# Kernel optimization log

Hardware: AMD Instinct MI355X
Metric: run time of the kernel (lower is better)

The kernel has to match this reference:

```python
import jax, jax.numpy as jnp
import numpy as np

N_NODES = 50000
N_EDGES = 800000
IN_F = 191
H1, C1 = 16, 16   # conv1: heads=16, out=16, concat -> 256
H2, C2 = 8, 3     # conv2: heads=8, out=3, concat=False -> mean


def _glorot(key, shape):
    fan = shape[0] + shape[-1] if len(shape) == 2 else sum(shape)
    s = jnp.sqrt(6.0 / fan)
    return jax.random.uniform(key, shape, jnp.float32, -s, s)


def setup_inputs() -> dict:
    key = jax.random.key(0)
    ks = jax.random.split(key, 16)
    x = jax.random.normal(ks[0], (N_NODES, IN_F), jnp.float32)
    edge_index = jax.random.randint(ks[1], (2, N_EDGES), 0, N_NODES)
    edge_attr = jax.random.normal(ks[2], (N_EDGES, 1), jnp.float32)
    return {
        "x": x, "edge_index": edge_index, "edge_attr": edge_attr,
        "W1": _glorot(ks[3], (IN_F, H1 * C1)),
        "We1": _glorot(ks[4], (1, H1 * C1)),
        "a_src1": _glorot(ks[5], (H1, C1)),
        "a_dst1": _glorot(ks[6], (H1, C1)),
        "a_edge1": _glorot(ks[7], (H1, C1)),
        "b1": jnp.zeros((H1 * C1,), jnp.float32),
        "W2": _glorot(ks[8], (H1 * C1, H2 * C2)),
        "We2": _glorot(ks[9], (1, H2 * C2)),
        "a_src2": _glorot(ks[10], (H2, C2)),
        "a_dst2": _glorot(ks[11], (H2, C2)),
        "a_edge2": _glorot(ks[12], (H2, C2)),
        "b2": jnp.zeros((C2,), jnp.float32),
    }


def gat_conv(x, src, dst, edge_attr, W, We, a_src, a_dst, a_edge, bias, H, C, concat):
    # x: [N, F]; src/dst: [E'] (self loops already appended); edge_attr: [E', De]
    N = x.shape[0]
    xl = (x @ W).reshape(N, H, C)                       # [N,H,C]
    e = (edge_attr @ We).reshape(-1, H, C)              # [E',H,C]
    alpha_src = (xl * a_src).sum(-1)                    # [N,H]
    alpha_dst = (xl * a_dst).sum(-1)                    # [N,H]
    alpha_e = (e * a_edge).sum(-1)                      # [E',H]
    alpha = alpha_src[src] + alpha_dst[dst] + alpha_e   # [E',H]
    alpha = jax.nn.leaky_relu(alpha, 0.2)
    # softmax over incoming edges per destination node
    m = jax.ops.segment_max(alpha, dst, num_segments=N)
    alpha = jnp.exp(alpha - m[dst])
    den = jax.ops.segment_sum(alpha, dst, num_segments=N)
    alpha = alpha / (den[dst] + 1e-16)
    out = jax.ops.segment_sum(alpha[:, :, None] * xl[src], dst, num_segments=N)  # [N,H,C]
    if concat:
        return out.reshape(N, H * C) + bias
    return out.mean(axis=1) + bias


def reference(x, edge_index, edge_attr, W1, We1, a_src1, a_dst1, a_edge1, b1,
              W2, We2, a_src2, a_dst2, a_edge2, b2):
    N = x.shape[0]
    # add self loops (PyG default, edge_attr fill_value='mean')
    loop = jnp.arange(N)
    src = jnp.concatenate([edge_index[0], loop])
    dst = jnp.concatenate([edge_index[1], loop])
    ea_mean = edge_attr.mean(axis=0, keepdims=True)
    ea = jnp.concatenate([edge_attr, jnp.broadcast_to(ea_mean, (N, edge_attr.shape[1]))], axis=0)

    h = gat_conv(x, src, dst, ea, W1, We1, a_src1, a_dst1, a_edge1, b1, H1, C1, True)
    h = jax.nn.elu(h)
    h = gat_conv(h, src, dst, ea, W2, We2, a_src2, a_dst2, a_edge2, b2, H2, C2, False)
    h = jax.nn.elu(h)
    return h
```

## Files before the change

### kernel.cpp

```cpp
#include <hip/hip_runtime.h>
#include <math.h>
#include <stdint.h>

#define N_NODES 50000
#define N_EDGES 800000
#define N_TOT   850000
#define IN_F    191
#define F1      256
#define NH1     16
#define NC1     16
#define F2      24
#define NH2     8
#define NC2     3
#define KP      192
#define MPAD    50048
#define NCVT_X  (MPAD * 24)
#define NCVT_W  (F1 * 24)

typedef __attribute__((ext_vector_type(8))) short bf16x8;
typedef __attribute__((ext_vector_type(4))) float f32x4;

#define GLL16(g, s) __builtin_amdgcn_global_load_lds( \
    (const __attribute__((address_space(1))) void*)(g), \
    (__attribute__((address_space(3))) void*)(s), 16, 0, 0)

__device__ __forceinline__ float lrelu(float x) { return x > 0.f ? x : 0.2f * x; }

__device__ __forceinline__ uint16_t f2bf1(float f) {
    uint32_t u = __float_as_uint(f);
    return (uint16_t)((u + 0x7fffu + ((u >> 16) & 1u)) >> 16);
}
__device__ __forceinline__ uint16_t f2bf(float f, float* back) {
    uint32_t u = __float_as_uint(f);
    uint32_t r = (u + 0x7fffu + ((u >> 16) & 1u)) >> 16;
    *back = __uint_as_float(r << 16);
    return (uint16_t)r;
}
__device__ __forceinline__ void bf2f2(uint32_t u, float* lo, float* hi) {
    *lo = __uint_as_float(u << 16);
    *hi = __uint_as_float(u & 0xffff0000u);
}

__global__ void k_hist(const int* __restrict__ ei, int* counts) {
    int e = blockIdx.x * blockDim.x + threadIdx.x;
    if (e < N_EDGES) atomicAdd(&counts[ei[N_EDGES + e]], 1);
}

__global__ void k_easum(const float* __restrict__ ea, float* scalars) {
    __shared__ float wsums[4];
    int t = threadIdx.x;
    float v = 0.f;
    for (int e = blockIdx.x * 256 + t; e < N_EDGES; e += 256 * 256) v += ea[e];
    #pragma unroll
    for (int off = 32; off >= 1; off >>= 1) v += __shfl_xor(v, off);
    if ((t & 63) == 0) wsums[t >> 6] = v;
    __syncthreads();
    if (t == 0) atomicAdd(&scalars[25], wsums[0] + wsums[1] + wsums[2] + wsums[3]);
}

__global__ void k_wedot(const float* __restrict__ We1, const float* __restrict__ ae1,
                        const float* __restrict__ We2, const float* __restrict__ ae2,
                        float* scalars) {
    int t = threadIdx.x;
    if (t < NH1) {
        float s = 0.f;
        for (int c = 0; c < NC1; c++) s += We1[t * NC1 + c] * ae1[t * NC1 + c];
        scalars[1 + t] = s;
    } else if (t < NH1 + NH2) {
        int h = t - NH1;
        float s = 0.f;
        for (int c = 0; c < NC2; c++) s += We2[h * NC2 + c] * ae2[h * NC2 + c];
        scalars[17 + h] = s;
    } else if (t == 63) {
        scalars[0] = scalars[25] / (float)N_EDGES;
    }
}

__global__ __launch_bounds__(1024) void k_scan1(const int* __restrict__ counts,
                                                int* rowptr, int* bsums) {
    __shared__ int wsum[16];
    int t = threadIdx.x;
    int lane = t & 63, w = t >> 6;
    int i = blockIdx.x * 1024 + t;
    int v = (i < N_NODES) ? counts[i] + 1 : 0;
    int incl = v;
    #pragma unroll
    for (int off = 1; off < 64; off <<= 1) {
        int u = __shfl_up(incl, off);
        if (lane >= off) incl += u;
    }
    if (lane == 63) wsum[w] = incl;
    __syncthreads();
    int woff = 0;
    #pragma unroll
    for (int k = 0; k < 16; k++) woff += (k < w) ? wsum[k] : 0;
    if (i < N_NODES) rowptr[i] = woff + incl - v;
    if (t == 1023) bsums[blockIdx.x] = woff + incl;
}

__global__ __launch_bounds__(1024) void k_scan2(int* rowptr, int* cursor,
                                                const int* __restrict__ bsums) {
    __shared__ int off_s;
    int b = blockIdx.x, t = threadIdx.x;
    if (t == 0) {
        int o = 0;
        for (int k = 0; k < b; k++) o += bsums[k];
        off_s = o;
        if (b == 48) rowptr[N_NODES] = o + bsums[48];
    }
    __syncthreads();
    int i = b * 1024 + t;
    if (i < N_NODES) {
        int r = rowptr[i] + off_s;
        rowptr[i] = r;
        cursor[i] = r;
    }
}

__global__ void k_scatter(const int* __restrict__ ei, const float* __restrict__ ea,
                          const float* __restrict__ scalars, int* cursor,
                          uint32_t* __restrict__ csr) {
    int i = blockIdx.x * blockDim.x + threadIdx.x;
    if (i < N_EDGES) {
        int s = ei[i], d = ei[N_EDGES + i];
        int pos = atomicAdd(&cursor[d], 1);
        csr[pos] = (uint32_t)s | ((uint32_t)f2bf1(ea[i]) << 16);
    } else if (i < N_TOT) {
        int n = i - N_EDGES;
        int pos = atomicAdd(&cursor[n], 1);
        csr[pos] = (uint32_t)n | ((uint32_t)f2bf1(scalars[0]) << 16);
    }
}

__global__ void k_cvt(const float* __restrict__ x, const float* __restrict__ W1,
                      uint16_t* __restrict__ xh, uint16_t* __restrict__ xl,
                      uint16_t* __restrict__ wht, uint16_t* __restrict__ wlt) {
    int idx = blockIdx.x * 256 + threadIdx.x;
    if (idx < NCVT_X) {
        int row = idx / 24, kw = idx - row * 24;
        int k0 = kw * 8;
        uint16_t hv[8], lv[8];
        #pragma unroll
        for (int j = 0; j < 8; j++) {
            int k = k0 + j;
            float v = (row < N_NODES && k < IN_F) ? x[(size_t)row * IN_F + k] : 0.f;
            float hf;
            hv[j] = f2bf(v, &hf);
            lv[j] = f2bf1(v - hf);
        }
        *(uint4*)(xh + (size_t)row * KP + k0) = *(const uint4*)hv;
        *(uint4*)(xl + (size_t)row * KP + k0) = *(const uint4*)lv;
    } else if (idx < NCVT_X + NCVT_W) {
        int id2 = idx - NCVT_X;
        int col = id2 / 24, kw = id2 - col * 24;
        int k0 = kw * 8;
        uint16_t hv[8], lv[8];
        #pragma unroll
        for (int j = 0; j < 8; j++) {
            int k = k0 + j;
            float v = (k < IN_F) ? W1[(size_t)k * F1 + col] : 0.f;
            float hf;
            hv[j] = f2bf(v, &hf);
            lv[j] = f2bf1(v - hf);
        }
        *(uint4*)(wht + (size_t)col * KP + k0) = *(const uint4*)hv;
        *(uint4*)(wlt + (size_t)col * KP + k0) = *(const uint4*)lv;
    }
}

__global__ __launch_bounds__(256) void k_gemm1_mfma(const uint16_t* __restrict__ xh,
        const uint16_t* __restrict__ xl, const uint16_t* __restrict__ wht,
        const uint16_t* __restrict__ wlt, const float* __restrict__ a_src,
        const float* __restrict__ a_dst, uint16_t* __restrict__ xl1b,
        float* __restrict__ asrc1, float* __restrict__ adst1) {
    __shared__ uint16_t Ah[4 * 64 * 8];
    __shared__ uint16_t Al[4 * 64 * 8];
    __shared__ uint16_t Bh[16 * 64 * 8];
    __shared__ uint16_t Bl[16 * 64 * 8];
    const int t = threadIdx.x;
    const int l = t & 63, w = t >> 6;
    const int m0 = blockIdx.x * 64;
    const int lr = l & 15, lk = l >> 4;

    f32x4 acc[4][4];
    #pragma unroll
    for (int i = 0; i < 4; i++)
        #pragma unroll
        for (int j = 0; j < 4; j++)
            acc[i][j] = (f32x4){0.f, 0.f, 0.f, 0.f};

    for (int ks = 0; ks < 6; ks++) {
        const int kb = ks * 32 + lk * 8;
        #pragma unroll
        for (int ii = 0; ii < 10; ii++) {
            const int idx = w * 10 + ii;
            if (idx < 8) {
                const int f = idx >> 1;
                const uint16_t* src = ((idx & 1) ? xl : xh) + (size_t)(m0 + f * 16 + lr) * KP + kb;
                uint16_t* dst = ((idx & 1) ? Al : Ah) + f * 512;
                GLL16(src, dst);
            } else {
                const int tt = idx - 8;
                const int g = tt >> 1;
                const uint16_t* src = ((tt & 1) ? wlt : wht) + (size_t)(g * 16 + lr) * KP + kb;
                uint16_t* dst = ((tt & 1) ? Bl : Bh) + g * 512;
                GLL16(src, dst);
            }
        }
        __syncthreads();
        bf16x8 ah[4], al[4];
        #pragma unroll
        for (int i = 0; i < 4; i++) {
            ah[i] = *(const bf16x8*)(Ah + (i * 64 + l) * 8);
            al[i] = *(const bf16x8*)(Al + (i * 64 + l) * 8);
        }
        #pragma unroll
        for (int gq = 0; gq < 4; gq++) {
            const int g = w * 4 + gq;
            bf16x8 bh = *(const bf16x8*)(Bh + (g * 64 + l) * 8);
            bf16x8 bl = *(const bf16x8*)(Bl + (g * 64 + l) * 8);
            #pragma unroll
            for (int i = 0; i < 4; i++) {
                acc[i][gq] = __builtin_amdgcn_mfma_f32_16x16x32_bf16(ah[i], bh, acc[i][gq], 0, 0, 0);
                acc[i][gq] = __builtin_amdgcn_mfma_f32_16x16x32_bf16(ah[i], bl, acc[i][gq], 0, 0, 0);
                acc[i][gq] = __builtin_amdgcn_mfma_f32_16x16x32_bf16(al[i], bh, acc[i][gq], 0, 0, 0);
            }
        }
        __syncthreads();
    }
    float asv[4], adv[4];
    #pragma unroll
    for (int gq = 0; gq < 4; gq++) {
        int h = w * 4 + gq;
        asv[gq] = a_src[h * 16 + lr];
        adv[gq] = a_dst[h * 16 + lr];
    }
    #pragma unroll
    for (int i = 0; i < 4; i++) {
        #pragma unroll
        for (int r = 0; r < 4; r++) {
            const int gm = m0 + i * 16 + lk * 4 + r;
            if (gm < N_NODES) {
                #pragma unroll
                for (int gq = 0; gq < 4; gq++) {
                    const int h = w * 4 + gq;
                    const int gn = h * 16 + lr;
                    float v = acc[i][gq][r];
                    xl1b[(size_t)gm * F1 + gn] = f2bf1(v);
                    float vs = v * asv[gq];
                    float vd = v * adv[gq];
                    vs += __shfl_xor(vs, 1); vs += __shfl_xor(vs, 2);
                    vs += __shfl_xor(vs, 4); vs += __shfl_xor(vs, 8);
                    vd += __shfl_xor(vd, 1); vd += __shfl_xor(vd, 2);
                    vd += __shfl_xor(vd, 4); vd += __shfl_xor(vd, 8);
                    if (lr == 0) {
                        asrc1[gm * 16 + h] = vs;
                        adst1[gm * 16 + h] = vd;
                    }
                }
            }
        }
    }
}

__global__ __launch_bounds__(256) void k_agg1(const int* __restrict__ rowptr,
        const uint32_t* __restrict__ csr,
        const uint16_t* __restrict__ xl1b, const float* __restrict__ asrc,
        const float* __restrict__ adst, const float* __restrict__ scalars,
        const float* __restrict__ b1, uint16_t* __restrict__ h1b) {
    int node = blockIdx.x * 4 + (threadIdx.x >> 6);
    int lane = threadIdx.x & 63;
    int eg = lane >> 4, h = lane & 15;
    int r0 = rowptr[node], r1 = rowptr[node + 1];
    float ad = adst[node * 16 + h];
    float wd = scalars[1 + h];
    float den = 0.f;
    float acc[16];
    #pragma unroll
    for (int c = 0; c < 16; c++) acc[c] = 0.f;
    for (int j = r0 + eg; j < r1; j += 4) {
        uint32_t pk = csr[j];
        int s = (int)(pk & 0xFFFFu);
        float eav = __uint_as_float(pk & 0xFFFF0000u);
        float a = lrelu(asrc[s * 16 + h] + ad + eav * wd);
        float wgt = __expf(a);
        den += wgt;
        const uint4* xp = (const uint4*)(xl1b + (size_t)s * F1 + h * 16);
        uint4 u0 = xp[0], u1 = xp[1];
        float lo, hi;
        bf2f2(u0.x, &lo, &hi); acc[0] += wgt * lo;  acc[1] += wgt * hi;
        bf2f2(u0.y, &lo, &hi); acc[2] += wgt * lo;  acc[3] += wgt * hi;
        bf2f2(u0.z, &lo, &hi); acc[4] += wgt * lo;  acc[5] += wgt * hi;
        bf2f2(u0.w, &lo, &hi); acc[6] += wgt * lo;  acc[7] += wgt * hi;
        bf2f2(u1.x, &lo, &hi); acc[8] += wgt * lo;  acc[9] += wgt * hi;
        bf2f2(u1.y, &lo, &hi); acc[10] += wgt * lo; acc[11] += wgt * hi;
        bf2f2(u1.z, &lo, &hi); acc[12] += wgt * lo; acc[13] += wgt * hi;
        bf2f2(u1.w, &lo, &hi); acc[14] += wgt * lo; acc[15] += wgt * hi;
    }
    den += __shfl_xor(den, 16);
    den += __shfl_xor(den, 32);
    float inv = 1.f / (den + 1e-16f);
    #pragma unroll
    for (int c = 0; c < 16; c++) {
        acc[c] += __shfl_xor(acc[c], 16);
        acc[c] += __shfl_xor(acc[c], 32);
    }
    if (eg == 0) {
        uint32_t pk[8];
        #pragma unroll
        for (int q = 0; q < 8; q++) {
            float v0 = acc[2 * q] * inv + b1[h * 16 + 2 * q];
            float v1 = acc[2 * q + 1] * inv + b1[h * 16 + 2 * q + 1];
            v0 = v0 > 0.f ? v0 : expm1f(v0);
            v1 = v1 > 0.f ? v1 : expm1f(v1);
            pk[q] = (uint32_t)f2bf1(v0) | ((uint32_t)f2bf1(v1) << 16);
        }
        uint4* op = (uint4*)(h1b + (size_t)node * F1 + h * 16);
        op[0] = make_uint4(pk[0], pk[1], pk[2], pk[3]);
        op[1] = make_uint4(pk[4], pk[5], pk[6], pk[7]);
    }
}

__global__ __launch_bounds__(256) void k_layer2(const uint16_t* __restrict__ h1b,
        const float* __restrict__ W2, const float* __restrict__ a_src,
        const float* __restrict__ a_dst, uint16_t* __restrict__ xl2b,
        float* __restrict__ asrc, float* __restrict__ adst) {
    __shared__ float W2s[F2][258];
    int t = threadIdx.x;
    for (int i = t; i < 256 * F2; i += 256) {
        int k = i / F2, c = i - k * F2;
        W2s[c][k] = W2[i];
    }
    __syncthreads();
    int idx = blockIdx.x * 256 + t;
    if (idx >= N_NODES * NH2) return;
    int n = idx >> 3, h = idx & 7;
    int c0 = h * 3;
    const uint4* hp = (const uint4*)(h1b + (size_t)n * F1);
    float a0 = 0.f, a1 = 0.f, a2 = 0.f;
    #pragma unroll 4
    for (int q = 0; q < 32; q++) {
        uint4 u = hp[q];
        float f[8];
        bf2f2(u.x, &f[0], &f[1]);
        bf2f2(u.y, &f[2], &f[3]);
        bf2f2(u.z, &f[4], &f[5]);
        bf2f2(u.w, &f[6], &f[7]);
        #pragma unroll
        for (int j = 0; j < 8; j++) {
            int k = q * 8 + j;
            a0 += f[j] * W2s[c0][k];
            a1 += f[j] * W2s[c0 + 1][k];
            a2 += f[j] * W2s[c0 + 2][k];
        }
    }
    uint2 pk;
    pk.x = (uint32_t)f2bf1(a0) | ((uint32_t)f2bf1(a1) << 16);
    pk.y = (uint32_t)f2bf1(a2);
    *(uint2*)(xl2b + (size_t)idx * 4) = pk;
    asrc[idx] = a0 * a_src[h * 3 + 0] + a1 * a_src[h * 3 + 1] + a2 * a_src[h * 3 + 2];
    adst[idx] = a0 * a_dst[h * 3 + 0] + a1 * a_dst[h * 3 + 1] + a2 * a_dst[h * 3 + 2];
}

__global__ __launch_bounds__(256) void k_agg2(const int* __restrict__ rowptr,
        const uint32_t* __restrict__ csr,
        const uint16_t* __restrict__ xl2b, const float* __restrict__ asrc,
        const float* __restrict__ adst, const float* __restrict__ scalars,
        const float* __restrict__ b2, float* __restrict__ out) {
    int node = blockIdx.x * 4 + (threadIdx.x >> 6);
    int lane = threadIdx.x & 63;
    int eg = lane >> 3, h = lane & 7;
    int r0 = rowptr[node], r1 = rowptr[node + 1];
    float ad = adst[node * 8 + h];
    float wd = scalars[17 + h];
    float den = 0.f, a0 = 0.f, a1 = 0.f, a2 = 0.f;
    for (int j = r0 + eg; j < r1; j += 8) {
        uint32_t pk = csr[j];
        int s = (int)(pk & 0xFFFFu);
        float eav = __uint_as_float(pk & 0xFFFF0000u);
        float a = lrelu(asrc[s * 8 + h] + ad + eav * wd);
        float wgt = __expf(a);
        den += wgt;
        const uint2* xp = (const uint2*)(xl2b + ((size_t)s * 8 + h) * 4);
        uint2 u = xp[0];
        float x0, x1, x2, dummy;
        bf2f2(u.x, &x0, &x1);
        bf2f2(u.y, &x2, &dummy);
        a0 += wgt * x0;
        a1 += wgt * x1;
        a2 += wgt * x2;
    }
    den += __shfl_xor(den, 8); den += __shfl_xor(den, 16); den += __shfl_xor(den, 32);
    float inv = 1.f / (den + 1e-16f);
    a0 += __shfl_xor(a0, 8); a0 += __shfl_xor(a0, 16); a0 += __shfl_xor(a0, 32);
    a1 += __shfl_xor(a1, 8); a1 += __shfl_xor(a1, 16); a1 += __shfl_xor(a1, 32);
    a2 += __shfl_xor(a2, 8); a2 += __shfl_xor(a2, 16); a2 += __shfl_xor(a2, 32);
    a0 *= inv; a1 *= inv; a2 *= inv;
    a0 += __shfl_xor(a0, 1); a0 += __shfl_xor(a0, 2); a0 += __shfl_xor(a0, 4);
    a1 += __shfl_xor(a1, 1); a1 += __shfl_xor(a1, 2); a1 += __shfl_xor(a1, 4);
    a2 += __shfl_xor(a2, 1); a2 += __shfl_xor(a2, 2); a2 += __shfl_xor(a2, 4);
    if (lane == 0) {
        float v0 = a0 * 0.125f + b2[0];
        float v1 = a1 * 0.125f + b2[1];
        float v2 = a2 * 0.125f + b2[2];
        out[node * 3 + 0] = v0 > 0.f ? v0 : expm1f(v0);
        out[node * 3 + 1] = v1 > 0.f ? v1 : expm1f(v1);
        out[node * 3 + 2] = v2 > 0.f ? v2 : expm1f(v2);
    }
}

extern "C" void kernel_launch(void* const* d_in, const int* in_sizes, int n_in,
                              void* d_out, int out_size, void* d_ws, size_t ws_size,
                              hipStream_t stream) {
    const float* x       = (const float*)d_in[0];
    const int*   ei      = (const int*)d_in[1];
    const float* ea      = (const float*)d_in[2];
    const float* W1      = (const float*)d_in[3];
    const float* We1     = (const float*)d_in[4];
    const float* a_src1  = (const float*)d_in[5];
    const float* a_dst1  = (const float*)d_in[6];
    const float* a_edge1 = (const float*)d_in[7];
    const float* b1      = (const float*)d_in[8];
    const float* W2      = (const float*)d_in[9];
    const float* We2     = (const float*)d_in[10];
    const float* a_src2  = (const float*)d_in[11];
    const float* a_dst2  = (const float*)d_in[12];
    const float* a_edge2 = (const float*)d_in[13];
    const float* b2      = (const float*)d_in[14];
    float* out = (float*)d_out;

    char* ws = (char*)d_ws;
    size_t off = 0;
    auto alloc = [&](size_t nbytes) -> void* {
        void* p = ws + off;
        off = (off + nbytes + 255) & ~(size_t)255;
        return p;
    };
    uint16_t* xl1b  = (uint16_t*)alloc((size_t)N_NODES * F1 * 2);
    uint16_t* h1b   = (uint16_t*)alloc((size_t)N_NODES * F1 * 2);
    float* asrc1    = (float*)alloc((size_t)N_NODES * NH1 * 4);
    float* adst1    = (float*)alloc((size_t)N_NODES * NH1 * 4);
    uint16_t* xl2b  = (uint16_t*)alloc((size_t)N_NODES * 32 * 2);
    float* asrc2    = (float*)alloc((size_t)N_NODES * NH2 * 4);
    float* adst2    = (float*)alloc((size_t)N_NODES * NH2 * 4);
    int*   counts   = (int*)alloc((size_t)N_NODES * 4);
    int*   rowptr   = (int*)alloc((size_t)(N_NODES + 1) * 4);
    int*   cursor   = (int*)alloc((size_t)N_NODES * 4);
    int*   bsums    = (int*)alloc(64 * 4);
    uint32_t* csr   = (uint32_t*)alloc((size_t)N_TOT * 4);
    float* scalars  = (float*)alloc(128);
    uint16_t* wht   = (uint16_t*)alloc((size_t)F1 * KP * 2);
    uint16_t* wlt   = (uint16_t*)alloc((size_t)F1 * KP * 2);
    uint16_t* xh    = (uint16_t*)alloc((size_t)MPAD * KP * 2);
    uint16_t* xlo   = (uint16_t*)alloc((size_t)MPAD * KP * 2);

    hipMemsetAsync(counts, 0, (size_t)N_NODES * 4, stream);
    hipMemsetAsync(scalars, 0, 128, stream);
    hipLaunchKernelGGL(k_hist, dim3((N_EDGES + 255) / 256), dim3(256), 0, stream,
                       ei, counts);
    hipLaunchKernelGGL(k_easum, dim3(256), dim3(256), 0, stream, ea, scalars);
    hipLaunchKernelGGL(k_wedot, dim3(1), dim3(64), 0, stream,
                       We1, a_edge1, We2, a_edge2, scalars);
    hipLaunchKernelGGL(k_scan1, dim3(49), dim3(1024), 0, stream, counts, rowptr, bsums);
    hipLaunchKernelGGL(k_scan2, dim3(49), dim3(1024), 0, stream, rowptr, cursor, bsums);
    hipLaunchKernelGGL(k_scatter, dim3((N_TOT + 255) / 256), dim3(256), 0, stream,
                       ei, ea, scalars, cursor, csr);
    hipLaunchKernelGGL(k_cvt, dim3((NCVT_X + NCVT_W + 255) / 256), dim3(256), 0, stream,
                       x, W1, xh, xlo, wht, wlt);
    hipLaunchKernelGGL(k_gemm1_mfma, dim3(MPAD / 64), dim3(256), 0, stream,
                       xh, xlo, wht, wlt, a_src1, a_dst1, xl1b, asrc1, adst1);
    hipLaunchKernelGGL(k_agg1, dim3(N_NODES / 4), dim3(256), 0, stream,
                       rowptr, csr, xl1b, asrc1, adst1, scalars, b1, h1b);
    hipLaunchKernelGGL(k_layer2, dim3((N_NODES * NH2 + 255) / 256), dim3(256), 0, stream,
                       h1b, W2, a_src2, a_dst2, xl2b, asrc2, adst2);
    hipLaunchKernelGGL(k_agg2, dim3(N_NODES / 4), dim3(256), 0, stream,
                       rowptr, csr, xl2b, asrc2, adst2, scalars, b2, out);
}
```

Baseline: 328.3 us.

## Drop split-bf16 GEMM, retile to 128x128, compute attention logits separately

Stops using the hi/lo bf16 split, so the layer-1 GEMM issues a single MFMA instead of three and the conversion kernel no longer writes or stores the low-part arrays. The GEMM is retiled to 128x128 blocks on a 2D grid. The attention-logit dot products move into a new kernel that reads the bf16 GEMM output. The edge-attribute mean now goes through per-block partial sums instead of an atomic, which also removes one memset. The cost is lower precision in the projection and the logits, plus an extra launch that rereads xl1b.

```diff
diff --git a/kernel.cpp b/kernel.cpp
--- a/kernel.cpp
+++ b/kernel.cpp
@@ -30,12 +30,6 @@
     uint32_t u = __float_as_uint(f);
     return (uint16_t)((u + 0x7fffu + ((u >> 16) & 1u)) >> 16);
 }
-__device__ __forceinline__ uint16_t f2bf(float f, float* back) {
-    uint32_t u = __float_as_uint(f);
-    uint32_t r = (u + 0x7fffu + ((u >> 16) & 1u)) >> 16;
-    *back = __uint_as_float(r << 16);
-    return (uint16_t)r;
-}
 __device__ __forceinline__ void bf2f2(uint32_t u, float* lo, float* hi) {
     *lo = __uint_as_float(u << 16);
     *hi = __uint_as_float(u & 0xffff0000u);
@@ -46,7 +40,7 @@
     if (e < N_EDGES) atomicAdd(&counts[ei[N_EDGES + e]], 1);
 }
 
-__global__ void k_easum(const float* __restrict__ ea, float* scalars) {
+__global__ void k_easum(const float* __restrict__ ea, float* __restrict__ part) {
     __shared__ float wsums[4];
     int t = threadIdx.x;
     float v = 0.f;
@@ -55,12 +49,12 @@
     for (int off = 32; off >= 1; off >>= 1) v += __shfl_xor(v, off);
     if ((t & 63) == 0) wsums[t >> 6] = v;
     __syncthreads();
-    if (t == 0) atomicAdd(&scalars[25], wsums[0] + wsums[1] + wsums[2] + wsums[3]);
+    if (t == 0) part[blockIdx.x] = wsums[0] + wsums[1] + wsums[2] + wsums[3];
 }
 
 __global__ void k_wedot(const float* __restrict__ We1, const float* __restrict__ ae1,
                         const float* __restrict__ We2, const float* __restrict__ ae2,
-                        float* scalars) {
+                        const float* __restrict__ part, float* scalars) {
     int t = threadIdx.x;
     if (t < NH1) {
         float s = 0.f;
@@ -71,9 +65,11 @@
         float s = 0.f;
         for (int c = 0; c < NC2; c++) s += We2[h * NC2 + c] * ae2[h * NC2 + c];
         scalars[17 + h] = s;
-    } else if (t == 63) {
-        scalars[0] = scalars[25] / (float)N_EDGES;
-    }
+    }
+    float v = part[t * 4] + part[t * 4 + 1] + part[t * 4 + 2] + part[t * 4 + 3];
+    #pragma unroll
+    for (int off = 32; off >= 1; off >>= 1) v += __shfl_xor(v, off);
+    if (t == 0) scalars[0] = v / (float)N_EDGES;
 }
 
 __global__ __launch_bounds__(1024) void k_scan1(const int* __restrict__ counts,
@@ -133,53 +129,43 @@
 }
 
 __global__ void k_cvt(const float* __restrict__ x, const float* __restrict__ W1,
-                      uint16_t* __restrict__ xh, uint16_t* __restrict__ xl,
-                      uint16_t* __restrict__ wht, uint16_t* __restrict__ wlt) {
+                      uint16_t* __restrict__ xh, uint16_t* __restrict__ wht) {
     int idx = blockIdx.x * 256 + threadIdx.x;
     if (idx < NCVT_X) {
         int row = idx / 24, kw = idx - row * 24;
         int k0 = kw * 8;
-        uint16_t hv[8], lv[8];
+        uint16_t hv[8];
         #pragma unroll
         for (int j = 0; j < 8; j++) {
             int k = k0 + j;
             float v = (row < N_NODES && k < IN_F) ? x[(size_t)row * IN_F + k] : 0.f;
-            float hf;
-            hv[j] = f2bf(v, &hf);
-            lv[j] = f2bf1(v - hf);
+            hv[j] = f2bf1(v);
         }
         *(uint4*)(xh + (size_t)row * KP + k0) = *(const uint4*)hv;
-        *(uint4*)(xl + (size_t)row * KP + k0) = *(const uint4*)lv;
     } else if (idx < NCVT_X + NCVT_W) {
         int id2 = idx - NCVT_X;
         int col = id2 / 24, kw = id2 - col * 24;
         int k0 = kw * 8;
-        uint16_t hv[8], lv[8];
+        uint16_t hv[8];
         #pragma unroll
         for (int j = 0; j < 8; j++) {
             int k = k0 + j;
             float v = (k < IN_F) ? W1[(size_t)k * F1 + col] : 0.f;
-            float hf;
-            hv[j] = f2bf(v, &hf);
-            lv[j] = f2bf1(v - hf);
+            hv[j] = f2bf1(v);
         }
         *(uint4*)(wht + (size_t)col * KP + k0) = *(const uint4*)hv;
-        *(uint4*)(wlt + (size_t)col * KP + k0) = *(const uint4*)lv;
     }
 }
 
 __global__ __launch_bounds__(256) void k_gemm1_mfma(const uint16_t* __restrict__ xh,
-        const uint16_t* __restrict__ xl, const uint16_t* __restrict__ wht,
-        const uint16_t* __restrict__ wlt, const float* __restrict__ a_src,
-        const float* __restrict__ a_dst, uint16_t* __restrict__ xl1b,
-        float* __restrict__ asrc1, float* __restrict__ adst1) {
-    __shared__ uint16_t Ah[4 * 64 * 8];
-    __shared__ uint16_t Al[4 * 64 * 8];
-    __shared__ uint16_t Bh[16 * 64 * 8];
-    __shared__ uint16_t Bl[16 * 64 * 8];
+        const uint16_t* __restrict__ wht, uint16_t* __restrict__ xl1b) {
+    __shared__ uint16_t ldsA[8 * 64 * 8];
+    __shared__ uint16_t ldsB[8 * 64 * 8];
     const int t = threadIdx.x;
     const int l = t & 63, w = t >> 6;
-    const int m0 = blockIdx.x * 64;
+    const int wm = w >> 1, wn = w & 1;
+    const int m0 = blockIdx.x * 128;
+    const int n0 = blockIdx.y * 128;
     const int lr = l & 15, lk = l >> 4;
 
     f32x4 acc[4][4];
@@ -192,75 +178,67 @@
     for (int ks = 0; ks < 6; ks++) {
         const int kb = ks * 32 + lk * 8;
         #pragma unroll
-        for (int ii = 0; ii < 10; ii++) {
-            const int idx = w * 10 + ii;
+        for (int ii = 0; ii < 4; ii++) {
+            const int idx = w * 4 + ii;
             if (idx < 8) {
-                const int f = idx >> 1;
-                const uint16_t* src = ((idx & 1) ? xl : xh) + (size_t)(m0 + f * 16 + lr) * KP + kb;
-                uint16_t* dst = ((idx & 1) ? Al : Ah) + f * 512;
-                GLL16(src, dst);
+                const uint16_t* src = xh + (size_t)(m0 + idx * 16 + lr) * KP + kb;
+                GLL16(src, ldsA + idx * 512);
             } else {
-                const int tt = idx - 8;
-                const int g = tt >> 1;
-                const uint16_t* src = ((tt & 1) ? wlt : wht) + (size_t)(g * 16 + lr) * KP + kb;
-                uint16_t* dst = ((tt & 1) ? Bl : Bh) + g * 512;
-                GLL16(src, dst);
+                const int g = idx - 8;
+                const uint16_t* src = wht + (size_t)(n0 + g * 16 + lr) * KP + kb;
+                GLL16(src, ldsB + g * 512);
             }
         }
         __syncthreads();
-        bf16x8 ah[4], al[4];
-        #pragma unroll
-        for (int i = 0; i < 4; i++) {
-            ah[i] = *(const bf16x8*)(Ah + (i * 64 + l) * 8);
-            al[i] = *(const bf16x8*)(Al + (i * 64 + l) * 8);
-        }
-        #pragma unroll
-        for (int gq = 0; gq < 4; gq++) {
-            const int g = w * 4 + gq;
-            bf16x8 bh = *(const bf16x8*)(Bh + (g * 64 + l) * 8);
-            bf16x8 bl = *(const bf16x8*)(Bl + (g * 64 + l) * 8);
+        bf16x8 ah[4];
+        #pragma unroll
+        for (int i = 0; i < 4; i++)
+            ah[i] = *(const bf16x8*)(ldsA + ((wm * 4 + i) * 64 + l) * 8);
+        #pragma unroll
+        for (int j = 0; j < 4; j++) {
+            bf16x8 bh = *(const bf16x8*)(ldsB + ((wn * 4 + j) * 64 + l) * 8);
             #pragma unroll
-            for (int i = 0; i < 4; i++) {
-                acc[i][gq] = __builtin_amdgcn_mfma_f32_16x16x32_bf16(ah[i], bh, acc[i][gq], 0, 0, 0);
-                acc[i][gq] = __builtin_amdgcn_mfma_f32_16x16x32_bf16(ah[i], bl, acc[i][gq], 0, 0, 0);
-                acc[i][gq] = __builtin_amdgcn_mfma_f32_16x16x32_bf16(al[i], bh, acc[i][gq], 0, 0, 0);
-            }
+            for (int i = 0; i < 4; i++)
+                acc[i][j] = __builtin_amdgcn_mfma_f32_16x16x32_bf16(ah[i], bh, acc[i][j], 0, 0, 0);
         }
         __syncthreads();
     }
-    float asv[4], adv[4];
-    #pragma unroll
-    for (int gq = 0; gq < 4; gq++) {
-        int h = w * 4 + gq;
-        asv[gq] = a_src[h * 16 + lr];
-        adv[gq] = a_dst[h * 16 + lr];
-    }
     #pragma unroll
     for (int i = 0; i < 4; i++) {
+        const int gm_base = m0 + wm * 64 + i * 16 + lk * 4;
         #pragma unroll
         for (int r = 0; r < 4; r++) {
-            const int gm = m0 + i * 16 + lk * 4 + r;
+            const int gm = gm_base + r;
             if (gm < N_NODES) {
                 #pragma unroll
-                for (int gq = 0; gq < 4; gq++) {
-                    const int h = w * 4 + gq;
-                    const int gn = h * 16 + lr;
-                    float v = acc[i][gq][r];
-                    xl1b[(size_t)gm * F1 + gn] = f2bf1(v);
-                    float vs = v * asv[gq];
-                    float vd = v * adv[gq];
-                    vs += __shfl_xor(vs, 1); vs += __shfl_xor(vs, 2);
-                    vs += __shfl_xor(vs, 4); vs += __shfl_xor(vs, 8);
-                    vd += __shfl_xor(vd, 1); vd += __shfl_xor(vd, 2);
-                    vd += __shfl_xor(vd, 4); vd += __shfl_xor(vd, 8);
-                    if (lr == 0) {
-                        asrc1[gm * 16 + h] = vs;
-                        adst1[gm * 16 + h] = vd;
-                    }
+                for (int j = 0; j < 4; j++) {
+                    const int gn = n0 + wn * 64 + j * 16 + lr;
+                    xl1b[(size_t)gm * F1 + gn] = f2bf1(acc[i][j][r]);
                 }
             }
         }
     }
+}
+
+__global__ void k_alphas1(const uint16_t* __restrict__ xl1b, const float* __restrict__ a_src,
+                          const float* __restrict__ a_dst,
+                          float* __restrict__ asrc, float* __restrict__ adst) {
+    int idx = blockIdx.x * blockDim.x + threadIdx.x;
+    if (idx >= N_NODES * NH1) return;
+    int h = idx & 15;
+    const uint4* xp = (const uint4*)(xl1b + (size_t)idx * 16);
+    uint4 u0 = xp[0], u1 = xp[1];
+    uint32_t us[8] = {u0.x, u0.y, u0.z, u0.w, u1.x, u1.y, u1.z, u1.w};
+    float as = 0.f, ad = 0.f;
+    #pragma unroll
+    for (int q = 0; q < 8; q++) {
+        float lo, hi;
+        bf2f2(us[q], &lo, &hi);
+        as += lo * a_src[h * 16 + 2 * q] + hi * a_src[h * 16 + 2 * q + 1];
+        ad += lo * a_dst[h * 16 + 2 * q] + hi * a_dst[h * 16 + 2 * q + 1];
+    }
+    asrc[idx] = as;
+    adst[idx] = ad;
 }
 
 __global__ __launch_bounds__(256) void k_agg1(const int* __restrict__ rowptr,
@@ -449,26 +427,26 @@
     int*   bsums    = (int*)alloc(64 * 4);
     uint32_t* csr   = (uint32_t*)alloc((size_t)N_TOT * 4);
     float* scalars  = (float*)alloc(128);
+    float* part     = (float*)alloc(256 * 4);
     uint16_t* wht   = (uint16_t*)alloc((size_t)F1 * KP * 2);
-    uint16_t* wlt   = (uint16_t*)alloc((size_t)F1 * KP * 2);
     uint16_t* xh    = (uint16_t*)alloc((size_t)MPAD * KP * 2);
-    uint16_t* xlo   = (uint16_t*)alloc((size_t)MPAD * KP * 2);
 
     hipMemsetAsync(counts, 0, (size_t)N_NODES * 4, stream);
-    hipMemsetAsync(scalars, 0, 128, stream);
     hipLaunchKernelGGL(k_hist, dim3((N_EDGES + 255) / 256), dim3(256), 0, stream,
                        ei, counts);
-    hipLaunchKernelGGL(k_easum, dim3(256), dim3(256), 0, stream, ea, scalars);
+    hipLaunchKernelGGL(k_easum, dim3(256), dim3(256), 0, stream, ea, part);
     hipLaunchKernelGGL(k_wedot, dim3(1), dim3(64), 0, stream,
-                       We1, a_edge1, We2, a_edge2, scalars);
+                       We1, a_edge1, We2, a_edge2, part, scalars);
     hipLaunchKernelGGL(k_scan1, dim3(49), dim3(1024), 0, stream, counts, rowptr, bsums);
     hipLaunchKernelGGL(k_scan2, dim3(49), dim3(1024), 0, stream, rowptr, cursor, bsums);
     hipLaunchKernelGGL(k_scatter, dim3((N_TOT + 255) / 256), dim3(256), 0, stream,
                        ei, ea, scalars, cursor, csr);
     hipLaunchKernelGGL(k_cvt, dim3((NCVT_X + NCVT_W + 255) / 256), dim3(256), 0, stream,
-                       x, W1, xh, xlo, wht, wlt);
-    hipLaunchKernelGGL(k_gemm1_mfma, dim3(MPAD / 64), dim3(256), 0, stream,
-                       xh, xlo, wht, wlt, a_src1, a_dst1, xl1b, asrc1, adst1);
+                       x, W1, xh, wht);
+    hipLaunchKernelGGL(k_gemm1_mfma, dim3(MPAD / 128, 2), dim3(256), 0, stream,
+                       xh, wht, xl1b);
+    hipLaunchKernelGGL(k_alphas1, dim3((N_NODES * NH1 + 255) / 256), dim3(256), 0, stream,
+                       xl1b, a_src1, a_dst1, asrc1, adst1);
     hipLaunchKernelGGL(k_agg1, dim3(N_NODES / 4), dim3(256), 0, stream,
                        rowptr, csr, xl1b, asrc1, adst1, scalars, b1, h1b);
     hipLaunchKernelGGL(k_layer2, dim3((N_NODES * NH2 + 255) / 256), dim3(256), 0, stream,
```

New measurement: 296.3 us. 9.7% less time.
